# Optimization experiments

Hardware: AMD Instinct MI355X
Metric: run time of the kernel (lower is better)

Reference implementation:

```python
import jax, jax.numpy as jnp
import numpy as np

N = 512   # memory_units == batch (module broadcasting requires B == N)
M = 256   # memory_unit_size
A = 128   # action_size
HS = 512  # hidden_size
C = 512   # controller_size


def setup_inputs() -> dict:
    key = jax.random.key(0)
    ks = jax.random.split(key, 20)
    s = 0.02  # small init keeps softplus(gamma)~0.7 so w**gamma stays stable
    d = {
        'action': jax.random.normal(ks[0], (N, A), jnp.float32),
        'hidden_state': jax.random.normal(ks[1], (N, HS), jnp.float32),
        'prev_read_weight': jax.random.uniform(ks[2], (N, N), jnp.float32),
        'prev_write_weight': jax.random.uniform(ks[3], (N, N), jnp.float32),
        'memory': jax.random.normal(ks[4], (N, M), jnp.float32),
        # GRU (single layer, single step, h0 = 0)
        'W_ih': jax.random.normal(ks[5], (3 * C, A + HS), jnp.float32) * s,
        'W_hh': jax.random.normal(ks[6], (3 * C, C), jnp.float32) * s,
        'b_ih': jnp.zeros((3 * C,), jnp.float32),
        'b_hh': jnp.zeros((3 * C,), jnp.float32),
        # heads
        'W_read': jax.random.normal(ks[7], (M, C), jnp.float32) * s,
        'b_read': jnp.zeros((M,), jnp.float32),
        'W_write': jax.random.normal(ks[8], (M, C), jnp.float32) * s,
        'b_write': jnp.zeros((M,), jnp.float32),
        'W_shift': jax.random.normal(ks[9], (N, C), jnp.float32) * s,
        'b_shift': jnp.zeros((N,), jnp.float32),
        'W_gamma': jax.random.normal(ks[10], (1, C), jnp.float32) * s,
        'b_gamma': jnp.zeros((1,), jnp.float32),
        'W_gate': jax.random.normal(ks[11], (1, C), jnp.float32) * s,
        'b_gate': jnp.zeros((1,), jnp.float32),
    }
    return d


def _lin(x, W, b):
    return x @ W.T + b


def _content_weight(key, memory):
    # cosine similarity then softmax over dim=1 (the batch/column axis),
    # exactly as in the torch source
    k = key / (jnp.linalg.norm(key, axis=1, keepdims=True) + 1e-16)
    m = memory / (jnp.linalg.norm(memory, axis=1, keepdims=True) + 1e-16)
    sim = m @ k.T  # [N, B]
    return jax.nn.softmax(sim, axis=1)


def reference(action, hidden_state, prev_read_weight, prev_write_weight, memory,
              W_ih, W_hh, b_ih, b_hh,
              W_read, b_read, W_write, b_write,
              W_shift, b_shift, W_gamma, b_gamma, W_gate, b_gate):
    # ---- GRU, one step, h0 = 0 (so h @ W_hh = 0, only b_hh contributes) ----
    x = jnp.concatenate([action, hidden_state], axis=1)      # [B, A+HS]
    gi = x @ W_ih.T + b_ih                                    # [B, 3C]
    gr, gz, gn = jnp.split(gi, 3, axis=1)
    hr, hz, hn = jnp.split(b_hh, 3)
    r = jax.nn.sigmoid(gr + hr)
    z = jax.nn.sigmoid(gz + hz)
    n = jnp.tanh(gn + r * hn)
    h = (1.0 - z) * n                                         # controller_out [B, C]

    # ---- content addressing ----
    read_key = _lin(h, W_read, b_read)                        # [B, M]
    write_key = _lin(h, W_write, b_write)
    rw = _content_weight(read_key, memory)                    # [N, B]
    ww = _content_weight(write_key, memory)

    # ---- interpolation gate (broadcast [B,1] against [N,B], valid since B==N) ----
    g = jax.nn.sigmoid(_lin(h, W_gate, b_gate))               # [B, 1]
    rw = g * rw + (1.0 - g) * prev_read_weight
    ww = g * ww + (1.0 - g) * prev_write_weight

    # ---- circular convolution: result[i,b] = sum_j w[(i-j)%N, b] * s[j, b] ----
    shift = jax.nn.softmax(_lin(h, W_shift, b_shift), axis=1)  # [B, N]
    ar = jnp.arange(N)
    idx = (ar[:, None] - ar[None, :]) % N                      # [N, N] circulant index

    def circ(w):
        return jnp.einsum('ijb,jb->ib', w[idx], shift)         # [N, B]

    # ---- sharpen: w ** gamma (gamma [B,1] broadcast, B==N), normalize over dim 0 ----
    gamma = jax.nn.softplus(_lin(h, W_gamma, b_gamma))         # [B, 1]

    def sharpen(w):
        wp = w ** gamma
        return wp / jnp.sum(wp, axis=0, keepdims=True)

    rw = sharpen(circ(rw))
    ww = sharpen(circ(ww))

    read_vector = rw @ memory                                  # [N, M] (pre-write memory)
    return (read_vector, rw, ww)
```

## Files before the change

kernel.cpp:

```cpp
#include <hip/hip_runtime.h>
#include <math.h>

#define N   512
#define M   256
#define A   128
#define HS  512
#define C   512

#define WS_H       0
#define WS_HEADS   262144
#define WS_SIMR    786432
#define WS_SIMW    1048576
#define WS_SHIFT   1310720
#define WS_WGRT    1572864
#define WS_WGWT    1835008
#define WS_SHIFTT  2097152
#define WS_CIRCTR  2359296
#define WS_CIRCTW  2621440
#define WS_MEMTS   2883584
#define WS_G       3014656
#define WS_GAMMA   3015168
#define WS_INVM    3015680
#define WS_INVKR   3016192
#define WS_INVKW   3016704
#define WS_CSR     3017216
#define WS_CSW     3017728
#define WS_XS      0
#define WS_GI      786432

#define LD4(p) (*reinterpret_cast<const float4*>(p))
#define LD2(p) (*reinterpret_cast<const float2*>(p))

typedef short bf16x8 __attribute__((ext_vector_type(8)));
typedef float f32x16 __attribute__((ext_vector_type(16)));

struct HiLo { bf16x8 hi, lo; };

__device__ __forceinline__ HiLo split8(const float4 u, const float4 v) {
  const float x[8] = {u.x, u.y, u.z, u.w, v.x, v.y, v.z, v.w};
  union { unsigned int w[4]; bf16x8 v; } H, L;
#pragma unroll
  for (int d = 0; d < 4; ++d) {
    const unsigned int a = __float_as_uint(x[2 * d]);
    const unsigned int b = __float_as_uint(x[2 * d + 1]);
    H.w[d] = (a >> 16) | (b & 0xFFFF0000u);
    const float la = x[2 * d]     - __uint_as_float(a & 0xFFFF0000u);
    const float lb = x[2 * d + 1] - __uint_as_float(b & 0xFFFF0000u);
    L.w[d] = (__float_as_uint(la) >> 16) | (__float_as_uint(lb) & 0xFFFF0000u);
  }
  HiLo r; r.hi = H.v; r.lo = L.v;
  return r;
}

__device__ __forceinline__ HiLo reint8(const float4 q0, const float4 q1) {
  HiLo r;
  r.hi = *reinterpret_cast<const bf16x8*>(&q0);
  r.lo = *reinterpret_cast<const bf16x8*>(&q1);
  return r;
}

__device__ __forceinline__ f32x16 mm3(const HiLo& a, const HiLo& b, f32x16 acc) {
  acc = __builtin_amdgcn_mfma_f32_32x32x16_bf16(a.hi, b.hi, acc, 0, 0, 0);
  acc = __builtin_amdgcn_mfma_f32_32x32x16_bf16(a.hi, b.lo, acc, 0, 0, 0);
  acc = __builtin_amdgcn_mfma_f32_32x32x16_bf16(a.lo, b.hi, acc, 0, 0, 0);
  return acc;
}

template <int NK, bool SA, bool SB>
__device__ __forceinline__ f32x16 tileMM(const float* __restrict__ pa,
                                         const float* __restrict__ pb) {
  f32x16 acc;
#pragma unroll
  for (int t = 0; t < 16; ++t) acc[t] = 0.0f;
  float4 aE0 = LD4(pa), aE1 = LD4(pa + 4);
  float4 bE0 = LD4(pb), bE1 = LD4(pb + 4);
  float4 aO0, aO1, bO0, bO1;
  if (NK > 1) {
    aO0 = LD4(pa + 16); aO1 = LD4(pa + 20);
    bO0 = LD4(pb + 16); bO1 = LD4(pb + 20);
  }
#pragma unroll
  for (int ks = 0; ks < NK; ++ks) {
    HiLo Af, Bf;
    if ((ks & 1) == 0) {
      Af = SA ? reint8(aE0, aE1) : split8(aE0, aE1);
      Bf = SB ? reint8(bE0, bE1) : split8(bE0, bE1);
      if (ks + 2 < NK) {
        const int k = (ks + 2) * 16;
        aE0 = LD4(pa + k); aE1 = LD4(pa + k + 4);
        bE0 = LD4(pb + k); bE1 = LD4(pb + k + 4);
      }
    } else {
      Af = SA ? reint8(aO0, aO1) : split8(aO0, aO1);
      Bf = SB ? reint8(bO0, bO1) : split8(bO0, bO1);
      if (ks + 2 < NK) {
        const int k = (ks + 2) * 16;
        aO0 = LD4(pa + k); aO1 = LD4(pa + k + 4);
        bO0 = LD4(pb + k); bO1 = LD4(pb + k + 4);
      }
    }
    acc = mm3(Af, Bf, acc);
  }
  return acc;
}

#define ACC_ROW(t, lane) (((t) & 3) + 8 * ((t) >> 2) + 4 * ((lane) >> 5))

__global__ __launch_bounds__(256) void k_prep(const float* __restrict__ action,
                                              const float* __restrict__ hidden,
                                              float* __restrict__ xs) {
  const int idx = blockIdx.x * 256 + threadIdx.x;
  const int row = idx / 80, g = idx % 80;
  const float* src = (g < 16) ? (action + row * 128 + g * 8)
                              : (hidden + row * 512 + (g - 16) * 8);
  const HiLo s = split8(LD4(src), LD4(src + 4));
  *reinterpret_cast<float4*>(xs + idx * 8)     = *reinterpret_cast<const float4*>(&s.hi);
  *reinterpret_cast<float4*>(xs + idx * 8 + 4) = *reinterpret_cast<const float4*>(&s.lo);
}

__global__ __launch_bounds__(256) void k_memT(const float* __restrict__ mem,
                                              float* __restrict__ memTs) {
  __shared__ float tile[32][33];
  const int bx = blockIdx.x, by = blockIdx.y, tx = threadIdx.x, ty = threadIdx.y;
#pragma unroll
  for (int k2 = 0; k2 < 4; ++k2)
    tile[ty + 8 * k2][tx] = mem[(by * 32 + ty + 8 * k2) * 256 + bx * 32 + tx];
  __syncthreads();
  if (ty < 4) {
    float4 q0, q1;
    q0.x = tile[8 * ty + 0][tx]; q0.y = tile[8 * ty + 1][tx];
    q0.z = tile[8 * ty + 2][tx]; q0.w = tile[8 * ty + 3][tx];
    q1.x = tile[8 * ty + 4][tx]; q1.y = tile[8 * ty + 5][tx];
    q1.z = tile[8 * ty + 6][tx]; q1.w = tile[8 * ty + 7][tx];
    const HiLo s = split8(q0, q1);
    float* dst = memTs + (bx * 32 + tx) * 512 + (by * 4 + ty) * 8;
    *reinterpret_cast<float4*>(dst)     = *reinterpret_cast<const float4*>(&s.hi);
    *reinterpret_cast<float4*>(dst + 4) = *reinterpret_cast<const float4*>(&s.lo);
  }
}

__global__ __launch_bounds__(64) void k_ggemm(const float* __restrict__ xs,
                                              const float* __restrict__ W_ih,
                                              float* __restrict__ gi) {
  const int lane = threadIdx.x;
  const int wg = blockIdx.x;
  const int xcd = wg & 7, inner = wg >> 3;
  const int bi = inner & 15;
  const int bc = xcd * 6 + (inner >> 4);
  const int r0 = bi * 32, c0 = bc * 32;
  const int m = lane & 31, koff = (lane >> 5) * 8;
  const f32x16 acc = tileMM<40, true, false>(xs + (r0 + m) * 640 + koff,
                                             W_ih + (c0 + m) * 640 + koff);
  const int col = c0 + m;
#pragma unroll
  for (int t = 0; t < 16; ++t)
    gi[(r0 + ACC_ROW(t, lane)) * 1536 + col] = acc[t];
}

__global__ __launch_bounds__(256) void k_act(const float* __restrict__ gi,
                                             const float* __restrict__ b_ih,
                                             const float* __restrict__ b_hh,
                                             float* __restrict__ h) {
  const int idx = blockIdx.x * 256 + threadIdx.x;
  const int b = idx >> 7, c4 = (idx & 127) * 4;
  const float4 g0 = LD4(gi + b * 1536 + c4);
  const float4 g1 = LD4(gi + b * 1536 + 512 + c4);
  const float4 g2 = LD4(gi + b * 1536 + 1024 + c4);
  const float4 bi0 = LD4(b_ih + c4);
  const float4 bi1 = LD4(b_ih + 512 + c4);
  const float4 bi2 = LD4(b_ih + 1024 + c4);
  const float4 bh0 = LD4(b_hh + c4);
  const float4 bh1 = LD4(b_hh + 512 + c4);
  const float4 bh2 = LD4(b_hh + 1024 + c4);
  const float gr[4] = {g0.x + bi0.x + bh0.x, g0.y + bi0.y + bh0.y, g0.z + bi0.z + bh0.z, g0.w + bi0.w + bh0.w};
  const float gz[4] = {g1.x + bi1.x + bh1.x, g1.y + bi1.y + bh1.y, g1.z + bi1.z + bh1.z, g1.w + bi1.w + bh1.w};
  const float gn[4] = {g2.x + bi2.x, g2.y + bi2.y, g2.z + bi2.z, g2.w + bi2.w};
  const float hn[4] = {bh2.x, bh2.y, bh2.z, bh2.w};
  float res[4];
#pragma unroll
  for (int u = 0; u < 4; ++u) {
    const float r = 1.0f / (1.0f + expf(-gr[u]));
    const float z = 1.0f / (1.0f + expf(-gz[u]));
    res[u] = (1.0f - z) * tanhf(gn[u] + r * hn[u]);
  }
  float4 o; o.x = res[0]; o.y = res[1]; o.z = res[2]; o.w = res[3];
  *reinterpret_cast<float4*>(h + b * 512 + c4) = o;
}

__global__ __launch_bounds__(64) void k_heads(const float* __restrict__ h,
                                              const float* __restrict__ W_read, const float* __restrict__ b_read,
                                              const float* __restrict__ W_write, const float* __restrict__ b_write,
                                              const float* __restrict__ W_shift, const float* __restrict__ b_shift,
                                              float* __restrict__ heads) {
  const int lane = threadIdx.x;
  const int wg = blockIdx.x;
  const int xcd = wg & 7, inner = wg >> 3;
  const int bi = inner & 15;
  const int bn = xcd * 4 + (inner >> 4);
  const int r0 = bi * 32, n0 = bn * 32;
  const float* W;
  const float* bias;
  if (n0 < 256)      { W = W_read  + n0 * 512;         bias = b_read  + n0; }
  else if (n0 < 512) { W = W_write + (n0 - 256) * 512; bias = b_write + (n0 - 256); }
  else               { W = W_shift + (n0 - 512) * 512; bias = b_shift + (n0 - 512); }
  const int m = lane & 31, koff = (lane >> 5) * 8;
  const f32x16 acc = tileMM<32, false, false>(h + (r0 + m) * 512 + koff,
                                              W + m * 512 + koff);
  const int col = lane & 31;
  const float bv = bias[col];
#pragma unroll
  for (int t = 0; t < 16; ++t)
    heads[(r0 + ACC_ROW(t, lane)) * 1024 + n0 + col] = acc[t] + bv;
}

__global__ __launch_bounds__(64) void k_ggnorms(const float* __restrict__ h,
                                                const float* __restrict__ W_gate, const float* __restrict__ b_gate,
                                                const float* __restrict__ W_gamma, const float* __restrict__ b_gamma,
                                                const float* __restrict__ memory,
                                                const float* __restrict__ heads,
                                                float* __restrict__ g, float* __restrict__ gamma,
                                                float* __restrict__ invm, float* __restrict__ invkr,
                                                float* __restrict__ invkw) {
  const int r = blockIdx.x, t = threadIdx.x;
  if (r < 512) {
    float ag = 0.f, am = 0.f;
#pragma unroll
    for (int u = 0; u < 8; ++u) {
      const float hv = h[r * 512 + t + 64 * u];
      ag = fmaf(hv, W_gate[t + 64 * u], ag);
      am = fmaf(hv, W_gamma[t + 64 * u], am);
    }
    for (int o = 32; o > 0; o >>= 1) { ag += __shfl_down(ag, o); am += __shfl_down(am, o); }
    if (t == 0) {
      g[r] = 1.0f / (1.0f + expf(-(ag + b_gate[0])));
      const float x = am + b_gamma[0];
      gamma[r] = (x > 0.f) ? (x + log1pf(expf(-x))) : log1pf(expf(x));
    }
    return;
  }
  float ss;
  float* dst;
  if (r < 1024) {
    const float4 v = LD4(memory + (r - 512) * 256 + t * 4);
    ss = v.x * v.x + v.y * v.y + v.z * v.z + v.w * v.w;
    dst = invm + (r - 512);
  } else {
    const int row = (r < 1536) ? (r - 1024) : (r - 1536);
    const int seg = (r < 1536) ? 0 : 256;
    const float4 v = LD4(heads + row * 1024 + seg + t * 4);
    ss = v.x * v.x + v.y * v.y + v.z * v.z + v.w * v.w;
    dst = ((r < 1536) ? invkr : invkw) + row;
  }
  for (int o = 32; o > 0; o >>= 1) ss += __shfl_down(ss, o);
  if (t == 0) *dst = 1.0f / (sqrtf(ss) + 1e-16f);
}

__global__ __launch_bounds__(64) void k_sim(const float* __restrict__ memory,
                                            const float* __restrict__ heads,
                                            float* __restrict__ simR, float* __restrict__ simW) {
  const int lane = threadIdx.x;
  const int i0 = blockIdx.x * 32;
  const int b0 = blockIdx.y * 32;
  const int seg = blockIdx.z ? 256 : 0;
  float* out = blockIdx.z ? simW : simR;
  const int m = lane & 31, koff = (lane >> 5) * 8;
  const f32x16 acc = tileMM<16, false, false>(memory + (i0 + m) * 256 + koff,
                                              heads + (b0 + m) * 1024 + seg + koff);
  const int col = lane & 31;
#pragma unroll
  for (int t = 0; t < 16; ++t)
    out[(i0 + ACC_ROW(t, lane)) * 512 + b0 + col] = acc[t];
}

__global__ __launch_bounds__(256) void k_rowsoft(const float* __restrict__ simR, const float* __restrict__ simW,
                                                 const float* __restrict__ heads,
                                                 const float* __restrict__ invm, const float* __restrict__ invkr,
                                                 const float* __restrict__ invkw, const float* __restrict__ g,
                                                 const float* __restrict__ prevR, const float* __restrict__ prevW,
                                                 float* __restrict__ wgr, float* __restrict__ wgw,
                                                 float* __restrict__ shift_nat) {
  __shared__ float red[8];
  const int row = blockIdx.x, mode = blockIdx.y, t = threadIdx.x;
  float v0, v1;
  if (mode == 2) {
    const float2 s = LD2(heads + row * 1024 + 512 + 2 * t);
    v0 = s.x; v1 = s.y;
  } else {
    const float* sim = mode ? simW : simR;
    const float* invk = mode ? invkw : invkr;
    const float2 s = LD2(sim + row * 512 + 2 * t);
    const float sc = invm[row];
    v0 = s.x * sc * invk[2 * t];
    v1 = s.y * sc * invk[2 * t + 1];
  }
  float mx = fmaxf(v0, v1);
  for (int o = 32; o > 0; o >>= 1) mx = fmaxf(mx, __shfl_down(mx, o));
  if ((t & 63) == 0) red[t >> 6] = mx;
  __syncthreads();
  mx = fmaxf(fmaxf(red[0], red[1]), fmaxf(red[2], red[3]));
  const float e0 = expf(v0 - mx), e1 = expf(v1 - mx);
  float s2 = e0 + e1;
  for (int o = 32; o > 0; o >>= 1) s2 += __shfl_down(s2, o);
  if ((t & 63) == 0) red[4 + (t >> 6)] = s2;
  __syncthreads();
  const float S = (red[4] + red[5]) + (red[6] + red[7]);
  const float inv = 1.0f / S;
  const float p0 = e0 * inv, p1 = e1 * inv;
  if (mode == 2) {
    *reinterpret_cast<float2*>(shift_nat + row * 512 + 2 * t) = make_float2(p0, p1);
  } else {
    const float* prev = mode ? prevW : prevR;
    float* outw = mode ? wgw : wgr;
    const float gv = g[row];
    const float2 pr = LD2(prev + row * 512 + 2 * t);
    *reinterpret_cast<float2*>(outw + row * 512 + 2 * t) =
        make_float2(gv * p0 + (1.0f - gv) * pr.x, gv * p1 + (1.0f - gv) * pr.y);
  }
}

__global__ __launch_bounds__(256) void k_transpose(const float* __restrict__ wgr, const float* __restrict__ wgw,
                                                   const float* __restrict__ shift_nat,
                                                   float* __restrict__ wgrT, float* __restrict__ wgwT,
                                                   float* __restrict__ shiftT) {
  __shared__ float tile[32][33];
  const int z = blockIdx.z;
  const float* src = (z == 0) ? wgr : (z == 1) ? wgw : shift_nat;
  float* dst = (z == 0) ? wgrT : (z == 1) ? wgwT : shiftT;
  const int bx = blockIdx.x, by = blockIdx.y, tx = threadIdx.x, ty = threadIdx.y;
#pragma unroll
  for (int k2 = 0; k2 < 4; ++k2)
    tile[ty + 8 * k2][tx] = src[(by * 32 + ty + 8 * k2) * 512 + bx * 32 + tx];
  __syncthreads();
#pragma unroll
  for (int k2 = 0; k2 < 4; ++k2)
    dst[(bx * 32 + ty + 8 * k2) * 512 + by * 32 + tx] = tile[tx][ty + 8 * k2];
}

__global__ __launch_bounds__(256) void k_circ(const float* __restrict__ wgrT, const float* __restrict__ wgwT,
                                              const float* __restrict__ shiftT,
                                              const float* __restrict__ gamma,
                                              float* __restrict__ circTR, float* __restrict__ circTW,
                                              float* __restrict__ csumR, float* __restrict__ csumW) {
  __shared__ float ls[4][1600];
  const int wid = threadIdx.x >> 6, lane = threadIdx.x & 63;
  const int b = blockIdx.x * 4 + wid;
  const float* wsrc = (blockIdx.y ? wgwT : wgrT) + b * 512;
  const float* ssrc = shiftT + b * 512;
  float* out = (blockIdx.y ? circTW : circTR) + b * 512;
  float* cs = blockIdx.y ? csumW : csumR;
  float* wl = ls[wid];
  float* sl = ls[wid] + 1056;

#pragma unroll
  for (int u = 0; u < 8; ++u) {
    const int k = lane + 64 * u;
    const float v = wsrc[k];
    wl[k + (k >> 5)] = v;
    const int k2 = k + 512;
    wl[k2 + (k2 >> 5)] = v;
    sl[k] = ssrc[k];
  }
  __syncthreads();

  const int i0 = lane * 8;
  float acc[8] = {};
  float win[8];
#pragma unroll
  for (int q = 0; q < 8; ++q) {
    const int a0 = i0 + 512 + q;
    win[q] = wl[a0 + (a0 >> 5)];
  }
  for (int jb = 0; jb < 512; jb += 8) {
    const float4 sA = LD4(&sl[jb]);
    const float4 sB = LD4(&sl[jb + 4]);
    const float sv[8] = {sA.x, sA.y, sA.z, sA.w, sB.x, sB.y, sB.z, sB.w};
#pragma unroll
    for (int u = 0; u < 8; ++u) {
      const float s = sv[u];
#pragma unroll
      for (int t = 0; t < 8; ++t) acc[t] = fmaf(win[(t - u) & 7], s, acc[t]);
      const int na = i0 + 511 - (jb + u);
      win[(7 - u) & 7] = wl[na + (na >> 5)];
    }
  }
  const float4 gm0 = LD4(gamma + i0);
  const float4 gm1 = LD4(gamma + i0 + 4);
  const float ge[8] = {gm0.x, gm0.y, gm0.z, gm0.w, gm1.x, gm1.y, gm1.z, gm1.w};
  float p[8];
  float local = 0.f;
#pragma unroll
  for (int q = 0; q < 8; ++q) { p[q] = powf(acc[q], ge[q]); local += p[q]; }
  *reinterpret_cast<float4*>(out + i0) = make_float4(p[0], p[1], p[2], p[3]);
  *reinterpret_cast<float4*>(out + i0 + 4) = make_float4(p[4], p[5], p[6], p[7]);
  for (int o = 32; o > 0; o >>= 1) local += __shfl_down(local, o);
  if (lane == 0) cs[b] = local;
}

__global__ __launch_bounds__(256) void k_finalw(const float* __restrict__ circTR, const float* __restrict__ circTW,
                                                const float* __restrict__ csumR, const float* __restrict__ csumW,
                                                float* __restrict__ d_out) {
  __shared__ float tile[32][33];
  const int z = blockIdx.z;
  const float* src = z ? circTW : circTR;
  const float* cs = z ? csumW : csumR;
  float* dst = d_out + 131072 + z * 262144;
  const int bx = blockIdx.x, by = blockIdx.y, tx = threadIdx.x, ty = threadIdx.y;
#pragma unroll
  for (int k2 = 0; k2 < 4; ++k2) {
    const int r = by * 32 + ty + 8 * k2;
    tile[ty + 8 * k2][tx] = src[r * 512 + bx * 32 + tx] * (1.0f / cs[r]);
  }
  __syncthreads();
#pragma unroll
  for (int k2 = 0; k2 < 4; ++k2)
    dst[(bx * 32 + ty + 8 * k2) * 512 + by * 32 + tx] = tile[tx][ty + 8 * k2];
}

__global__ __launch_bounds__(64) void k_readvec(const float* __restrict__ rw,
                                                const float* __restrict__ memTs,
                                                float* __restrict__ rv) {
  const int lane = threadIdx.x;
  const int i0 = blockIdx.x * 32;
  const int m0 = blockIdx.y * 32;
  const int kz = blockIdx.z * 256;
  const int m = lane & 31, koff = (lane >> 5) * 8;
  const f32x16 acc = tileMM<16, false, true>(rw + (i0 + m) * 512 + kz + koff,
                                             memTs + (m0 + m) * 512 + kz + koff);
  const int col = lane & 31;
#pragma unroll
  for (int t = 0; t < 16; ++t)
    atomicAdd(&rv[(i0 + ACC_ROW(t, lane)) * 256 + m0 + col], acc[t]);
}

extern "C" void kernel_launch(void* const* d_in, const int* in_sizes, int n_in,
                              void* d_out, int out_size, void* d_ws, size_t ws_size,
                              hipStream_t stream) {
  const float* action  = (const float*)d_in[0];
  const float* hidden  = (const float*)d_in[1];
  const float* prevR   = (const float*)d_in[2];
  const float* prevW   = (const float*)d_in[3];
  const float* memory  = (const float*)d_in[4];
  const float* W_ih    = (const float*)d_in[5];
  const float* b_ih    = (const float*)d_in[7];
  const float* b_hh    = (const float*)d_in[8];
  const float* W_read  = (const float*)d_in[9];
  const float* b_read  = (const float*)d_in[10];
  const float* W_write = (const float*)d_in[11];
  const float* b_write = (const float*)d_in[12];
  const float* W_shift = (const float*)d_in[13];
  const float* b_shift = (const float*)d_in[14];
  const float* W_gamma = (const float*)d_in[15];
  const float* b_gamma = (const float*)d_in[16];
  const float* W_gate  = (const float*)d_in[17];
  const float* b_gate  = (const float*)d_in[18];

  float* ws = (float*)d_ws;
  float* out = (float*)d_out;

  hipMemsetAsync(out, 0, 131072 * sizeof(float), stream);

  k_prep<<<160, 256, 0, stream>>>(action, hidden, ws + WS_XS);
  k_memT<<<dim3(8, 16), dim3(32, 8), 0, stream>>>(memory, ws + WS_MEMTS);
  k_ggemm<<<768, 64, 0, stream>>>(ws + WS_XS, W_ih, ws + WS_GI);
  k_act<<<256, 256, 0, stream>>>(ws + WS_GI, b_ih, b_hh, ws + WS_H);
  k_heads<<<512, 64, 0, stream>>>(ws + WS_H, W_read, b_read, W_write, b_write,
                                  W_shift, b_shift, ws + WS_HEADS);
  k_ggnorms<<<2048, 64, 0, stream>>>(ws + WS_H, W_gate, b_gate, W_gamma, b_gamma,
                                     memory, ws + WS_HEADS,
                                     ws + WS_G, ws + WS_GAMMA,
                                     ws + WS_INVM, ws + WS_INVKR, ws + WS_INVKW);
  k_sim<<<dim3(16, 16, 2), 64, 0, stream>>>(memory, ws + WS_HEADS, ws + WS_SIMR, ws + WS_SIMW);
  k_rowsoft<<<dim3(512, 3), 256, 0, stream>>>(ws + WS_SIMR, ws + WS_SIMW, ws + WS_HEADS,
                                              ws + WS_INVM, ws + WS_INVKR, ws + WS_INVKW,
                                              ws + WS_G, prevR, prevW,
                                              ws + WS_SIMR, ws + WS_SIMW, ws + WS_SHIFT);
  k_transpose<<<dim3(16, 16, 3), dim3(32, 8), 0, stream>>>(ws + WS_SIMR, ws + WS_SIMW, ws + WS_SHIFT,
                                                           ws + WS_WGRT, ws + WS_WGWT, ws + WS_SHIFTT);
  k_circ<<<dim3(128, 2), 256, 0, stream>>>(ws + WS_WGRT, ws + WS_WGWT, ws + WS_SHIFTT,
                                           ws + WS_GAMMA,
                                           ws + WS_CIRCTR, ws + WS_CIRCTW,
                                           ws + WS_CSR, ws + WS_CSW);
  k_finalw<<<dim3(16, 16, 2), dim3(32, 8), 0, stream>>>(ws + WS_CIRCTR, ws + WS_CIRCTW,
                                                        ws + WS_CSR, ws + WS_CSW, out);
  k_readvec<<<dim3(16, 8, 2), 64, 0, stream>>>(out + 131072, ws + WS_MEMTS, out);
}
```

Measured before the change: 183.5 us.

## Fuse pipeline stages to cut kernel launches and intermediate transposes

After: 180.9 us. Within noise of the previous version (-1.4%).

```diff
diff --git a/kernel.cpp b/kernel.cpp
--- a/kernel.cpp
+++ b/kernel.cpp
@@ -1,32 +1,20 @@
 #include <hip/hip_runtime.h>
 #include <math.h>
-
-#define N   512
-#define M   256
-#define A   128
-#define HS  512
-#define C   512
 
 #define WS_H       0
 #define WS_HEADS   262144
 #define WS_SIMR    786432
 #define WS_SIMW    1048576
-#define WS_SHIFT   1310720
-#define WS_WGRT    1572864
-#define WS_WGWT    1835008
-#define WS_SHIFTT  2097152
-#define WS_CIRCTR  2359296
-#define WS_CIRCTW  2621440
-#define WS_MEMTS   2883584
+#define WS_WGRT    1310720
+#define WS_WGWT    1572864
+#define WS_SHIFTT  1835008
+#define WS_MEMTS   2097152
+#define WS_GI      2228224
 #define WS_G       3014656
 #define WS_GAMMA   3015168
 #define WS_INVM    3015680
-#define WS_INVKR   3016192
-#define WS_INVKW   3016704
-#define WS_CSR     3017216
-#define WS_CSW     3017728
-#define WS_XS      0
-#define WS_GI      786432
+#define WS_SSR     3016192
+#define WS_SSW     3016704
 
 #define LD4(p) (*reinterpret_cast<const float4*>(p))
 #define LD2(p) (*reinterpret_cast<const float2*>(p))
@@ -68,10 +56,8 @@
 
 template <int NK, bool SA, bool SB>
 __device__ __forceinline__ f32x16 tileMM(const float* __restrict__ pa,
-                                         const float* __restrict__ pb) {
-  f32x16 acc;
-#pragma unroll
-  for (int t = 0; t < 16; ++t) acc[t] = 0.0f;
+                                         const float* __restrict__ pb,
+                                         f32x16 acc) {
   float4 aE0 = LD4(pa), aE1 = LD4(pa + 4);
   float4 bE0 = LD4(pb), bE1 = LD4(pb + 4);
   float4 aO0, aO1, bO0, bO1;
@@ -106,92 +92,114 @@
 
 #define ACC_ROW(t, lane) (((t) & 3) + 8 * ((t) >> 2) + 4 * ((lane) >> 5))
 
-__global__ __launch_bounds__(256) void k_prep(const float* __restrict__ action,
-                                              const float* __restrict__ hidden,
-                                              float* __restrict__ xs) {
-  const int idx = blockIdx.x * 256 + threadIdx.x;
-  const int row = idx / 80, g = idx % 80;
-  const float* src = (g < 16) ? (action + row * 128 + g * 8)
-                              : (hidden + row * 512 + (g - 16) * 8);
-  const HiLo s = split8(LD4(src), LD4(src + 4));
-  *reinterpret_cast<float4*>(xs + idx * 8)     = *reinterpret_cast<const float4*>(&s.hi);
-  *reinterpret_cast<float4*>(xs + idx * 8 + 4) = *reinterpret_cast<const float4*>(&s.lo);
-}
-
-__global__ __launch_bounds__(256) void k_memT(const float* __restrict__ mem,
-                                              float* __restrict__ memTs) {
+__global__ __launch_bounds__(64) void k_gmt(const float* __restrict__ action,
+                                            const float* __restrict__ hidden,
+                                            const float* __restrict__ W_ih,
+                                            const float* __restrict__ memory,
+                                            float* __restrict__ gi,
+                                            float* __restrict__ memTs,
+                                            float* __restrict__ invm) {
   __shared__ float tile[32][33];
-  const int bx = blockIdx.x, by = blockIdx.y, tx = threadIdx.x, ty = threadIdx.y;
-#pragma unroll
-  for (int k2 = 0; k2 < 4; ++k2)
-    tile[ty + 8 * k2][tx] = mem[(by * 32 + ty + 8 * k2) * 256 + bx * 32 + tx];
+  const int blk = blockIdx.x;
+  const int lane = threadIdx.x;
+  if (blk < 768) {
+    const int xcd = blk & 7, inner = blk >> 3;
+    const int bi = inner & 15;
+    const int bc = xcd * 6 + (inner >> 4);
+    const int r0 = bi * 32, c0 = bc * 32;
+    const int m = lane & 31, koff = (lane >> 5) * 8;
+    f32x16 acc;
+#pragma unroll
+    for (int t = 0; t < 16; ++t) acc[t] = 0.0f;
+    const float* Wrow = W_ih + (c0 + m) * 640 + koff;
+    acc = tileMM<8, false, false>(action + (r0 + m) * 128 + koff, Wrow, acc);
+    acc = tileMM<32, false, false>(hidden + (r0 + m) * 512 + koff, Wrow + 128, acc);
+    const int col = c0 + m;
+#pragma unroll
+    for (int t = 0; t < 16; ++t)
+      gi[(r0 + ACC_ROW(t, lane)) * 1536 + col] = acc[t];
+  } else if (blk < 896) {
+    const int tb = blk - 768;
+    const int bx = tb & 7, by = tb >> 3;
+    const int r = lane >> 1, cs = (lane & 1) * 16;
+#pragma unroll
+    for (int u = 0; u < 4; ++u) {
+      const float4 v = LD4(memory + (by * 32 + r) * 256 + bx * 32 + cs + 4 * u);
+      tile[r][cs + 4 * u + 0] = v.x;
+      tile[r][cs + 4 * u + 1] = v.y;
+      tile[r][cs + 4 * u + 2] = v.z;
+      tile[r][cs + 4 * u + 3] = v.w;
+    }
+    __syncthreads();
+    const int xx = lane >> 1, g2 = (lane & 1) * 2;
+#pragma unroll
+    for (int gd = 0; gd < 2; ++gd) {
+      const int gg = g2 + gd;
+      float4 q0, q1;
+      q0.x = tile[8 * gg + 0][xx]; q0.y = tile[8 * gg + 1][xx];
+      q0.z = tile[8 * gg + 2][xx]; q0.w = tile[8 * gg + 3][xx];
+      q1.x = tile[8 * gg + 4][xx]; q1.y = tile[8 * gg + 5][xx];
+      q1.z = tile[8 * gg + 6][xx]; q1.w = tile[8 * gg + 7][xx];
+      const HiLo s = split8(q0, q1);
+      float* dst = memTs + (bx * 32 + xx) * 512 + (by * 4 + gg) * 8;
+      *reinterpret_cast<float4*>(dst)     = *reinterpret_cast<const float4*>(&s.hi);
+      *reinterpret_cast<float4*>(dst + 4) = *reinterpret_cast<const float4*>(&s.lo);
+    }
+  } else {
+    const int row = blk - 896;
+    const float4 v = LD4(memory + row * 256 + lane * 4);
+    float ss = v.x * v.x + v.y * v.y + v.z * v.z + v.w * v.w;
+    for (int o = 32; o > 0; o >>= 1) ss += __shfl_down(ss, o);
+    if (lane == 0) invm[row] = 1.0f / (sqrtf(ss) + 1e-16f);
+  }
+}
+
+__global__ __launch_bounds__(256) void k_actgg(const float* __restrict__ gi,
+                                               const float* __restrict__ b_ih,
+                                               const float* __restrict__ b_hh,
+                                               const float* __restrict__ W_gate, const float* __restrict__ b_gate,
+                                               const float* __restrict__ W_gamma, const float* __restrict__ b_gamma,
+                                               float* __restrict__ h,
+                                               float* __restrict__ g, float* __restrict__ gamma,
+                                               float* __restrict__ ssr, float* __restrict__ ssw) {
+  __shared__ float red[8];
+  const int b = blockIdx.x, t = threadIdx.x;
+  float hv[2];
+#pragma unroll
+  for (int u = 0; u < 2; ++u) {
+    const int c = t + u * 256;
+    const float gr = gi[b * 1536 + c] + b_ih[c] + b_hh[c];
+    const float gz = gi[b * 1536 + 512 + c] + b_ih[512 + c] + b_hh[512 + c];
+    const float gn = gi[b * 1536 + 1024 + c] + b_ih[1024 + c];
+    const float hn = b_hh[1024 + c];
+    const float r = 1.0f / (1.0f + expf(-gr));
+    const float z = 1.0f / (1.0f + expf(-gz));
+    hv[u] = (1.0f - z) * tanhf(gn + r * hn);
+    h[b * 512 + c] = hv[u];
+  }
+  float ag = hv[0] * W_gate[t] + hv[1] * W_gate[t + 256];
+  float am = hv[0] * W_gamma[t] + hv[1] * W_gamma[t + 256];
+  for (int o = 32; o > 0; o >>= 1) { ag += __shfl_down(ag, o); am += __shfl_down(am, o); }
+  const int wid = t >> 6, lane = t & 63;
+  if (lane == 0) { red[wid] = ag; red[4 + wid] = am; }
   __syncthreads();
-  if (ty < 4) {
-    float4 q0, q1;
-    q0.x = tile[8 * ty + 0][tx]; q0.y = tile[8 * ty + 1][tx];
-    q0.z = tile[8 * ty + 2][tx]; q0.w = tile[8 * ty + 3][tx];
-    q1.x = tile[8 * ty + 4][tx]; q1.y = tile[8 * ty + 5][tx];
-    q1.z = tile[8 * ty + 6][tx]; q1.w = tile[8 * ty + 7][tx];
-    const HiLo s = split8(q0, q1);
-    float* dst = memTs + (bx * 32 + tx) * 512 + (by * 4 + ty) * 8;
-    *reinterpret_cast<float4*>(dst)     = *reinterpret_cast<const float4*>(&s.hi);
-    *reinterpret_cast<float4*>(dst + 4) = *reinterpret_cast<const float4*>(&s.lo);
-  }
-}
-
-__global__ __launch_bounds__(64) void k_ggemm(const float* __restrict__ xs,
-                                              const float* __restrict__ W_ih,
-                                              float* __restrict__ gi) {
-  const int lane = threadIdx.x;
-  const int wg = blockIdx.x;
-  const int xcd = wg & 7, inner = wg >> 3;
-  const int bi = inner & 15;
-  const int bc = xcd * 6 + (inner >> 4);
-  const int r0 = bi * 32, c0 = bc * 32;
-  const int m = lane & 31, koff = (lane >> 5) * 8;
-  const f32x16 acc = tileMM<40, true, false>(xs + (r0 + m) * 640 + koff,
-                                             W_ih + (c0 + m) * 640 + koff);
-  const int col = c0 + m;
-#pragma unroll
-  for (int t = 0; t < 16; ++t)
-    gi[(r0 + ACC_ROW(t, lane)) * 1536 + col] = acc[t];
-}
-
-__global__ __launch_bounds__(256) void k_act(const float* __restrict__ gi,
-                                             const float* __restrict__ b_ih,
-                                             const float* __restrict__ b_hh,
-                                             float* __restrict__ h) {
-  const int idx = blockIdx.x * 256 + threadIdx.x;
-  const int b = idx >> 7, c4 = (idx & 127) * 4;
-  const float4 g0 = LD4(gi + b * 1536 + c4);
-  const float4 g1 = LD4(gi + b * 1536 + 512 + c4);
-  const float4 g2 = LD4(gi + b * 1536 + 1024 + c4);
-  const float4 bi0 = LD4(b_ih + c4);
-  const float4 bi1 = LD4(b_ih + 512 + c4);
-  const float4 bi2 = LD4(b_ih + 1024 + c4);
-  const float4 bh0 = LD4(b_hh + c4);
-  const float4 bh1 = LD4(b_hh + 512 + c4);
-  const float4 bh2 = LD4(b_hh + 1024 + c4);
-  const float gr[4] = {g0.x + bi0.x + bh0.x, g0.y + bi0.y + bh0.y, g0.z + bi0.z + bh0.z, g0.w + bi0.w + bh0.w};
-  const float gz[4] = {g1.x + bi1.x + bh1.x, g1.y + bi1.y + bh1.y, g1.z + bi1.z + bh1.z, g1.w + bi1.w + bh1.w};
-  const float gn[4] = {g2.x + bi2.x, g2.y + bi2.y, g2.z + bi2.z, g2.w + bi2.w};
-  const float hn[4] = {bh2.x, bh2.y, bh2.z, bh2.w};
-  float res[4];
-#pragma unroll
-  for (int u = 0; u < 4; ++u) {
-    const float r = 1.0f / (1.0f + expf(-gr[u]));
-    const float z = 1.0f / (1.0f + expf(-gz[u]));
-    res[u] = (1.0f - z) * tanhf(gn[u] + r * hn[u]);
-  }
-  float4 o; o.x = res[0]; o.y = res[1]; o.z = res[2]; o.w = res[3];
-  *reinterpret_cast<float4*>(h + b * 512 + c4) = o;
+  if (t == 0) {
+    const float AG = (red[0] + red[1]) + (red[2] + red[3]);
+    const float AM = (red[4] + red[5]) + (red[6] + red[7]);
+    g[b] = 1.0f / (1.0f + expf(-(AG + b_gate[0])));
+    const float x = AM + b_gamma[0];
+    gamma[b] = (x > 0.f) ? (x + log1pf(expf(-x))) : log1pf(expf(x));
+    ssr[b] = 0.0f;
+    ssw[b] = 0.0f;
+  }
 }
 
 __global__ __launch_bounds__(64) void k_heads(const float* __restrict__ h,
                                               const float* __restrict__ W_read, const float* __restrict__ b_read,
                                               const float* __restrict__ W_write, const float* __restrict__ b_write,
                                               const float* __restrict__ W_shift, const float* __restrict__ b_shift,
-                                              float* __restrict__ heads) {
+                                              float* __restrict__ heads,
+                                              float* __restrict__ ssr, float* __restrict__ ssw) {
   const int lane = threadIdx.x;
   const int wg = blockIdx.x;
   const int xcd = wg & 7, inner = wg >> 3;
@@ -204,55 +212,27 @@
   else if (n0 < 512) { W = W_write + (n0 - 256) * 512; bias = b_write + (n0 - 256); }
   else               { W = W_shift + (n0 - 512) * 512; bias = b_shift + (n0 - 512); }
   const int m = lane & 31, koff = (lane >> 5) * 8;
-  const f32x16 acc = tileMM<32, false, false>(h + (r0 + m) * 512 + koff,
-                                              W + m * 512 + koff);
+  f32x16 acc;
+#pragma unroll
+  for (int t = 0; t < 16; ++t) acc[t] = 0.0f;
+  acc = tileMM<32, false, false>(h + (r0 + m) * 512 + koff, W + m * 512 + koff, acc);
   const int col = lane & 31;
   const float bv = bias[col];
 #pragma unroll
   for (int t = 0; t < 16; ++t)
     heads[(r0 + ACC_ROW(t, lane)) * 1024 + n0 + col] = acc[t] + bv;
-}
-
-__global__ __launch_bounds__(64) void k_ggnorms(const float* __restrict__ h,
-                                                const float* __restrict__ W_gate, const float* __restrict__ b_gate,
-                                                const float* __restrict__ W_gamma, const float* __restrict__ b_gamma,
-                                                const float* __restrict__ memory,
-                                                const float* __restrict__ heads,
-                                                float* __restrict__ g, float* __restrict__ gamma,
-                                                float* __restrict__ invm, float* __restrict__ invkr,
-                                                float* __restrict__ invkw) {
-  const int r = blockIdx.x, t = threadIdx.x;
-  if (r < 512) {
-    float ag = 0.f, am = 0.f;
-#pragma unroll
-    for (int u = 0; u < 8; ++u) {
-      const float hv = h[r * 512 + t + 64 * u];
-      ag = fmaf(hv, W_gate[t + 64 * u], ag);
-      am = fmaf(hv, W_gamma[t + 64 * u], am);
+  if (n0 < 512) {
+    float* ss = (n0 < 256) ? ssr : ssw;
+#pragma unroll
+    for (int t = 0; t < 16; ++t) {
+      const float v = acc[t] + bv;
+      float sq = v * v;
+      sq += __shfl_xor(sq, 1);  sq += __shfl_xor(sq, 2);
+      sq += __shfl_xor(sq, 4);  sq += __shfl_xor(sq, 8);
+      sq += __shfl_xor(sq, 16);
+      if ((lane & 31) == 0) atomicAdd(&ss[r0 + ACC_ROW(t, lane)], sq);
     }
-    for (int o = 32; o > 0; o >>= 1) { ag += __shfl_down(ag, o); am += __shfl_down(am, o); }
-    if (t == 0) {
-      g[r] = 1.0f / (1.0f + expf(-(ag + b_gate[0])));
-      const float x = am + b_gamma[0];
-      gamma[r] = (x > 0.f) ? (x + log1pf(expf(-x))) : log1pf(expf(x));
-    }
-    return;
-  }
-  float ss;
-  float* dst;
-  if (r < 1024) {
-    const float4 v = LD4(memory + (r - 512) * 256 + t * 4);
-    ss = v.x * v.x + v.y * v.y + v.z * v.z + v.w * v.w;
-    dst = invm + (r - 512);
-  } else {
-    const int row = (r < 1536) ? (r - 1024) : (r - 1536);
-    const int seg = (r < 1536) ? 0 : 256;
-    const float4 v = LD4(heads + row * 1024 + seg + t * 4);
-    ss = v.x * v.x + v.y * v.y + v.z * v.z + v.w * v.w;
-    dst = ((r < 1536) ? invkr : invkw) + row;
-  }
-  for (int o = 32; o > 0; o >>= 1) ss += __shfl_down(ss, o);
-  if (t == 0) *dst = 1.0f / (sqrtf(ss) + 1e-16f);
+  }
 }
 
 __global__ __launch_bounds__(64) void k_sim(const float* __restrict__ memory,
@@ -264,8 +244,11 @@
   const int seg = blockIdx.z ? 256 : 0;
   float* out = blockIdx.z ? simW : simR;
   const int m = lane & 31, koff = (lane >> 5) * 8;
-  const f32x16 acc = tileMM<16, false, false>(memory + (i0 + m) * 256 + koff,
-                                              heads + (b0 + m) * 1024 + seg + koff);
+  f32x16 acc;
+#pragma unroll
+  for (int t = 0; t < 16; ++t) acc[t] = 0.0f;
+  acc = tileMM<16, false, false>(memory + (i0 + m) * 256 + koff,
+                                 heads + (b0 + m) * 1024 + seg + koff, acc);
   const int col = lane & 31;
 #pragma unroll
   for (int t = 0; t < 16; ++t)
@@ -274,11 +257,12 @@
 
 __global__ __launch_bounds__(256) void k_rowsoft(const float* __restrict__ simR, const float* __restrict__ simW,
                                                  const float* __restrict__ heads,
-                                                 const float* __restrict__ invm, const float* __restrict__ invkr,
-                                                 const float* __restrict__ invkw, const float* __restrict__ g,
+                                                 const float* __restrict__ invm,
+                                                 const float* __restrict__ ssr, const float* __restrict__ ssw,
+                                                 const float* __restrict__ g,
                                                  const float* __restrict__ prevR, const float* __restrict__ prevW,
-                                                 float* __restrict__ wgr, float* __restrict__ wgw,
-                                                 float* __restrict__ shift_nat) {
+                                                 float* __restrict__ wgrT, float* __restrict__ wgwT,
+                                                 float* __restrict__ shiftT) {
   __shared__ float red[8];
   const int row = blockIdx.x, mode = blockIdx.y, t = threadIdx.x;
   float v0, v1;
@@ -287,11 +271,13 @@
     v0 = s.x; v1 = s.y;
   } else {
     const float* sim = mode ? simW : simR;
-    const float* invk = mode ? invkw : invkr;
+    const float* ss = mode ? ssw : ssr;
     const float2 s = LD2(sim + row * 512 + 2 * t);
     const float sc = invm[row];
-    v0 = s.x * sc * invk[2 * t];
-    v1 = s.y * sc * invk[2 * t + 1];
+    const float ik0 = 1.0f / (sqrtf(ss[2 * t]) + 1e-16f);
+    const float ik1 = 1.0f / (sqrtf(ss[2 * t + 1]) + 1e-16f);
+    v0 = s.x * sc * ik0;
+    v1 = s.y * sc * ik1;
   }
   float mx = fmaxf(v0, v1);
   for (int o = 32; o > 0; o >>= 1) mx = fmaxf(mx, __shfl_down(mx, o));
@@ -307,47 +293,27 @@
   const float inv = 1.0f / S;
   const float p0 = e0 * inv, p1 = e1 * inv;
   if (mode == 2) {
-    *reinterpret_cast<float2*>(shift_nat + row * 512 + 2 * t) = make_float2(p0, p1);
+    shiftT[(2 * t) * 512 + row]     = p0;
+    shiftT[(2 * t + 1) * 512 + row] = p1;
   } else {
     const float* prev = mode ? prevW : prevR;
-    float* outw = mode ? wgw : wgr;
+    float* outwT = mode ? wgwT : wgrT;
     const float gv = g[row];
     const float2 pr = LD2(prev + row * 512 + 2 * t);
-    *reinterpret_cast<float2*>(outw + row * 512 + 2 * t) =
-        make_float2(gv * p0 + (1.0f - gv) * pr.x, gv * p1 + (1.0f - gv) * pr.y);
-  }
-}
-
-__global__ __launch_bounds__(256) void k_transpose(const float* __restrict__ wgr, const float* __restrict__ wgw,
-                                                   const float* __restrict__ shift_nat,
-                                                   float* __restrict__ wgrT, float* __restrict__ wgwT,
-                                                   float* __restrict__ shiftT) {
-  __shared__ float tile[32][33];
-  const int z = blockIdx.z;
-  const float* src = (z == 0) ? wgr : (z == 1) ? wgw : shift_nat;
-  float* dst = (z == 0) ? wgrT : (z == 1) ? wgwT : shiftT;
-  const int bx = blockIdx.x, by = blockIdx.y, tx = threadIdx.x, ty = threadIdx.y;
-#pragma unroll
-  for (int k2 = 0; k2 < 4; ++k2)
-    tile[ty + 8 * k2][tx] = src[(by * 32 + ty + 8 * k2) * 512 + bx * 32 + tx];
-  __syncthreads();
-#pragma unroll
-  for (int k2 = 0; k2 < 4; ++k2)
-    dst[(bx * 32 + ty + 8 * k2) * 512 + by * 32 + tx] = tile[tx][ty + 8 * k2];
+    outwT[(2 * t) * 512 + row]     = gv * p0 + (1.0f - gv) * pr.x;
+    outwT[(2 * t + 1) * 512 + row] = gv * p1 + (1.0f - gv) * pr.y;
+  }
 }
 
 __global__ __launch_bounds__(256) void k_circ(const float* __restrict__ wgrT, const float* __restrict__ wgwT,
                                               const float* __restrict__ shiftT,
                                               const float* __restrict__ gamma,
-                                              float* __restrict__ circTR, float* __restrict__ circTW,
-                                              float* __restrict__ csumR, float* __restrict__ csumW) {
+                                              float* __restrict__ d_out) {
   __shared__ float ls[4][1600];
   const int wid = threadIdx.x >> 6, lane = threadIdx.x & 63;
   const int b = blockIdx.x * 4 + wid;
   const float* wsrc = (blockIdx.y ? wgwT : wgrT) + b * 512;
   const float* ssrc = shiftT + b * 512;
-  float* out = (blockIdx.y ? circTW : circTR) + b * 512;
-  float* cs = blockIdx.y ? csumW : csumR;
   float* wl = ls[wid];
   float* sl = ls[wid] + 1056;
 
@@ -390,30 +356,13 @@
   float local = 0.f;
 #pragma unroll
   for (int q = 0; q < 8; ++q) { p[q] = powf(acc[q], ge[q]); local += p[q]; }
-  *reinterpret_cast<float4*>(out + i0) = make_float4(p[0], p[1], p[2], p[3]);
-  *reinterpret_cast<float4*>(out + i0 + 4) = make_float4(p[4], p[5], p[6], p[7]);
   for (int o = 32; o > 0; o >>= 1) local += __shfl_down(local, o);
-  if (lane == 0) cs[b] = local;
-}
-
-__global__ __launch_bounds__(256) void k_finalw(const float* __restrict__ circTR, const float* __restrict__ circTW,
-                                                const float* __restrict__ csumR, const float* __restrict__ csumW,
-                                                float* __restrict__ d_out) {
-  __shared__ float tile[32][33];
-  const int z = blockIdx.z;
-  const float* src = z ? circTW : circTR;
-  const float* cs = z ? csumW : csumR;
-  float* dst = d_out + 131072 + z * 262144;
-  const int bx = blockIdx.x, by = blockIdx.y, tx = threadIdx.x, ty = threadIdx.y;
-#pragma unroll
-  for (int k2 = 0; k2 < 4; ++k2) {
-    const int r = by * 32 + ty + 8 * k2;
-    tile[ty + 8 * k2][tx] = src[r * 512 + bx * 32 + tx] * (1.0f / cs[r]);
-  }
-  __syncthreads();
-#pragma unroll
-  for (int k2 = 0; k2 < 4; ++k2)
-    dst[(bx * 32 + ty + 8 * k2) * 512 + by * 32 + tx] = tile[tx][ty + 8 * k2];
+  local = __shfl(local, 0);
+  const float inv = 1.0f / local;
+  float* dst = d_out + 131072 + (blockIdx.y ? 262144 : 0);
+#pragma unroll
+  for (int q = 0; q < 8; ++q)
+    dst[(i0 + q) * 512 + b] = p[q] * inv;
 }
 
 __global__ __launch_bounds__(64) void k_readvec(const float* __restrict__ rw,
@@ -422,14 +371,16 @@
   const int lane = threadIdx.x;
   const int i0 = blockIdx.x * 32;
   const int m0 = blockIdx.y * 32;
-  const int kz = blockIdx.z * 256;
   const int m = lane & 31, koff = (lane >> 5) * 8;
-  const f32x16 acc = tileMM<16, false, true>(rw + (i0 + m) * 512 + kz + koff,
-                                             memTs + (m0 + m) * 512 + kz + koff);
+  f32x16 acc;
+#pragma unroll
+  for (int t = 0; t < 16; ++t) acc[t] = 0.0f;
+  acc = tileMM<32, false, true>(rw + (i0 + m) * 512 + koff,
+                                memTs + (m0 + m) * 512 + koff, acc);
   const int col = lane & 31;
 #pragma unroll
   for (int t = 0; t < 16; ++t)
-    atomicAdd(&rv[(i0 + ACC_ROW(t, lane)) * 256 + m0 + col], acc[t]);
+    rv[(i0 + ACC_ROW(t, lane)) * 256 + m0 + col] = acc[t];
 }
 
 extern "C" void kernel_launch(void* const* d_in, const int* in_sizes, int n_in,
@@ -457,30 +408,21 @@
   float* ws = (float*)d_ws;
   float* out = (float*)d_out;
 
-  hipMemsetAsync(out, 0, 131072 * sizeof(float), stream);
-
-  k_prep<<<160, 256, 0, stream>>>(action, hidden, ws + WS_XS);
-  k_memT<<<dim3(8, 16), dim3(32, 8), 0, stream>>>(memory, ws + WS_MEMTS);
-  k_ggemm<<<768, 64, 0, stream>>>(ws + WS_XS, W_ih, ws + WS_GI);
-  k_act<<<256, 256, 0, stream>>>(ws + WS_GI, b_ih, b_hh, ws + WS_H);
+  k_gmt<<<1408, 64, 0, stream>>>(action, hidden, W_ih, memory,
+                                 ws + WS_GI, ws + WS_MEMTS, ws + WS_INVM);
+  k_actgg<<<512, 256, 0, stream>>>(ws + WS_GI, b_ih, b_hh,
+                                   W_gate, b_gate, W_gamma, b_gamma,
+                                   ws + WS_H, ws + WS_G, ws + WS_GAMMA,
+                                   ws + WS_SSR, ws + WS_SSW);
   k_heads<<<512, 64, 0, stream>>>(ws + WS_H, W_read, b_read, W_write, b_write,
-                                  W_shift, b_shift, ws + WS_HEADS);
-  k_ggnorms<<<2048, 64, 0, stream>>>(ws + WS_H, W_gate, b_gate, W_gamma, b_gamma,
-                                     memory, ws + WS_HEADS,
-                                     ws + WS_G, ws + WS_GAMMA,
-                                     ws + WS_INVM, ws + WS_INVKR, ws + WS_INVKW);
+                                  W_shift, b_shift, ws + WS_HEADS,
+                                  ws + WS_SSR, ws + WS_SSW);
   k_sim<<<dim3(16, 16, 2), 64, 0, stream>>>(memory, ws + WS_HEADS, ws + WS_SIMR, ws + WS_SIMW);
   k_rowsoft<<<dim3(512, 3), 256, 0, stream>>>(ws + WS_SIMR, ws + WS_SIMW, ws + WS_HEADS,
-                                              ws + WS_INVM, ws + WS_INVKR, ws + WS_INVKW,
+                                              ws + WS_INVM, ws + WS_SSR, ws + WS_SSW,
                                               ws + WS_G, prevR, prevW,
-                                              ws + WS_SIMR, ws + WS_SIMW, ws + WS_SHIFT);
-  k_transpose<<<dim3(16, 16, 3), dim3(32, 8), 0, stream>>>(ws + WS_SIMR, ws + WS_SIMW, ws + WS_SHIFT,
-                                                           ws + WS_WGRT, ws + WS_WGWT, ws + WS_SHIFTT);
+                                              ws + WS_WGRT, ws + WS_WGWT, ws + WS_SHIFTT);
   k_circ<<<dim3(128, 2), 256, 0, stream>>>(ws + WS_WGRT, ws + WS_WGWT, ws + WS_SHIFTT,
-                                           ws + WS_GAMMA,
-                                           ws + WS_CIRCTR, ws + WS_CIRCTW,
-                                           ws + WS_CSR, ws + WS_CSW);
-  k_finalw<<<dim3(16, 16, 2), dim3(32, 8), 0, stream>>>(ws + WS_CIRCTR, ws + WS_CIRCTW,
-                                                        ws + WS_CSR, ws + WS_CSW, out);
-  k_readvec<<<dim3(16, 8, 2), 64, 0, stream>>>(out + 131072, ws + WS_MEMTS, out);
-}
+                                           ws + WS_GAMMA, out);
+  k_readvec<<<dim3(16, 8), 64, 0, stream>>>(out + 131072, ws + WS_MEMTS, out);
+}
```
